# Optimization experiments

Hardware: AMD Instinct MI355X
Metric: run time of the kernel (lower is better)

Reference implementation:

```python
import jax, jax.numpy as jnp
import numpy as np

N_QUBITS = 12
DEPTH = 1
OUTPUT_DIM = 4096
BATCH = 2048
M = 4096  # input dim == 2**N_QUBITS, amplitude embedding needs no padding
EPS = 1e-10


def _rot_matrix(phi, theta, omega):
    """PennyLane qml.Rot(phi, theta, omega) = RZ(omega) @ RY(theta) @ RZ(phi)."""
    c = jnp.cos(theta * 0.5).astype(jnp.complex64)
    s = jnp.sin(theta * 0.5).astype(jnp.complex64)
    e_mm = jnp.exp(-0.5j * (phi + omega))  # e^{-i(phi+omega)/2}
    e_pm = jnp.exp(0.5j * (phi - omega))   # e^{+i(phi-omega)/2}
    e_mp = jnp.exp(0.5j * (omega - phi))   # e^{+i(omega-phi)/2}
    e_pp = jnp.exp(0.5j * (phi + omega))   # e^{+i(phi+omega)/2}
    return jnp.stack([
        jnp.stack([e_mm * c, -e_pm * s]),
        jnp.stack([e_mp * s, e_pp * c]),
    ])  # [2, 2] complex64


def _apply_1q(state, U, wire):
    """Apply 2x2 gate U on `wire` (MSB-first convention, as PennyLane)."""
    B = state.shape[0]
    s = state.reshape(B, 2 ** wire, 2, -1)
    return jnp.einsum('ij,bajc->baic', U, s).reshape(B, -1)


def _apply_cnot(state, ctrl, tgt):
    """Apply CNOT with control ctrl < target tgt (MSB-first wires)."""
    B = state.shape[0]
    s = state.reshape(B, 2 ** ctrl, 2, 2 ** (tgt - ctrl - 1), 2, -1)
    flipped = s[:, :, 1, :, ::-1, :]  # flip target axis where control == 1
    s = jnp.concatenate([s[:, :, :1], flipped[:, :, None]], axis=2)
    return s.reshape(B, -1)


def _circuit(x, w):
    # amplitude embedding: per-sample L2 normalize, uniform fallback for ~zero rows
    norm = jnp.linalg.norm(x, axis=1, keepdims=True)  # [B, 1]
    amp = jnp.where(norm > EPS, x / jnp.maximum(norm, EPS), 1.0 / np.sqrt(M))
    state = amp.astype(jnp.complex64)  # [B, 2^12]
    for layer in range(DEPTH):
        for i in range(N_QUBITS):
            U = _rot_matrix(w[layer, i, 0], w[layer, i, 1], w[layer, i, 2])
            state = _apply_1q(state, U, i)
        for i in range(N_QUBITS):
            for j in range(i + 1, N_QUBITS):
                state = _apply_cnot(state, i, j)
    probs = state.real ** 2 + state.imag ** 2  # [B, 4096]
    probs_n = probs[:, :OUTPUT_DIM]
    ps = probs_n.sum(axis=1, keepdims=True)
    out = jnp.where(ps > EPS, probs_n / jnp.maximum(ps, EPS), 1.0 / OUTPUT_DIM)
    return out.astype(jnp.float32)


def setup_inputs() -> dict:
    key = jax.random.key(0)
    k1, k2 = jax.random.split(key)
    x = jax.random.normal(k1, (BATCH, M), dtype=jnp.float32)
    quantum_weights = jax.random.uniform(
        k2, (DEPTH, N_QUBITS, 3), dtype=jnp.float32) * (2.0 * np.pi)
    return {"x": x, "quantum_weights": quantum_weights}


def reference(x, quantum_weights):
    return _circuit(x, quantum_weights)
```

## Files before the change

### kernel.cpp

```cpp
#include <hip/hip_runtime.h>
#include <math.h>


#define EPSF 1e-10f

__device__ __forceinline__ float dpp_xor1(float v) {
    return __int_as_float(__builtin_amdgcn_update_dpp(
        0, __float_as_int(v), 0xB1, 0xF, 0xF, true));
}
__device__ __forceinline__ float dpp_xor2(float v) {
    return __int_as_float(__builtin_amdgcn_update_dpp(
        0, __float_as_int(v), 0x4E, 0xF, 0xF, true));
}

__global__ __launch_bounds__(256, 4) void qdense_kernel(
    const float* __restrict__ x,
    const float* __restrict__ qw,
    float* __restrict__ out)
{
    __shared__ __align__(16) float buf[8192];
    __shared__ float bsum[4];

    const int tid = threadIdx.x;
    const int w   = tid >> 6;
    const int ln  = tid & 63;
    const int row = blockIdx.x;

    const float* __restrict__ xr = x + ((size_t)row << 12);

    float ar[16], ai[16];

    float ss = 0.f;
    const int wl = (w << 6) | ln;
#pragma unroll
    for (int l = 0; l < 16; ++l) {
        const float v = xr[(l << 8) | wl];
        ar[l] = v;
        ss = fmaf(v, v, ss);
    }
#pragma unroll
    for (int m = 32; m; m >>= 1) ss += __shfl_xor(ss, m, 64);
    if (ln == 0) bsum[w] = ss;
    __syncthreads();
    const float ss_tot = bsum[0] + bsum[1] + bsum[2] + bsum[3];

    const float nrm = sqrtf(ss_tot);
    if (nrm > EPSF) {
        const float inv = 1.0f / nrm;
#pragma unroll
        for (int l = 0; l < 16; ++l) ar[l] *= inv;
    } else {
#pragma unroll
        for (int l = 0; l < 16; ++l) ar[l] = 0.015625f;
    }
#pragma unroll
    for (int l = 0; l < 16; ++l) ai[l] = 0.f;

#define COEFFS(wq)                                                   \
    const float phi = qw[(wq) * 3 + 0];                              \
    const float th  = qw[(wq) * 3 + 1];                              \
    const float om  = qw[(wq) * 3 + 2];                              \
    const float c = __cosf(0.5f * th), s = __sinf(0.5f * th);        \
    const float A = 0.5f * (phi + om), Bb = 0.5f * (phi - om);       \
    const float p = c * __cosf(A), q = c * __sinf(A);                \
    const float r = s * __cosf(Bb), t = s * __sinf(Bb);

#pragma unroll
    for (int wq = 0; wq < 4; ++wq) {
        COEFFS(wq);
        const int bit = 1 << (3 - wq);
#pragma unroll
        for (int l0 = 0; l0 < 16; ++l0) {
            if (l0 & bit) continue;
            const int l1 = l0 | bit;
            const float a0r = ar[l0], a0i = ai[l0];
            const float a1r = ar[l1], a1i = ai[l1];
            ar[l0] =  p * a0r + q * a0i - r * a1r + t * a1i;
            ai[l0] = -q * a0r + p * a0i - t * a1r - r * a1i;
            ar[l1] =  r * a0r + t * a0i + p * a1r - q * a1i;
            ai[l1] = -t * a0r + r * a0i + q * a1r + p * a1i;
        }
    }

#pragma unroll
    for (int wq = 10; wq <= 11; ++wq) {
        COEFFS(wq);
        const int pb = 11 - wq;
        const int side = (ln >> pb) & 1;
        const float sq = side ? -q : q;
        const float sr = side ? r : -r;
#pragma unroll
        for (int l = 0; l < 16; ++l) {
            const float pr = (pb == 0) ? dpp_xor1(ar[l]) : dpp_xor2(ar[l]);
            const float pi = (pb == 0) ? dpp_xor1(ai[l]) : dpp_xor2(ai[l]);
            const float mr = ar[l], mi = ai[l];
            ar[l] = p * mr + sq * mi + sr * pr + t * pi;
            ai[l] = p * mi - sq * mr - t * pr + sr * pi;
        }
    }

    float2* __restrict__ B2 = reinterpret_cast<float2*>(buf);
#pragma unroll
    for (int l = 0; l < 16; ++l)
        B2[(l << 8) | (w << 6) | (ln ^ (l << 2))] = make_float2(ar[l], ai[l]);
    __syncthreads();
    {
        const int lo = (ln >> 2) & 15;
#pragma unroll
        for (int l2 = 0; l2 < 16; ++l2) {
            const int la = ((l2 << 2) | (ln & 3)) ^ (lo << 2);
            const float2 v = B2[(lo << 8) | (w << 6) | la];
            ar[l2] = v.x; ai[l2] = v.y;
        }
    }

#pragma unroll
    for (int wq = 6; wq < 10; ++wq) {
        COEFFS(wq);
        const int bit = 1 << (9 - wq);
#pragma unroll
        for (int l0 = 0; l0 < 16; ++l0) {
            if (l0 & bit) continue;
            const int l1 = l0 | bit;
            const float a0r = ar[l0], a0i = ai[l0];
            const float a1r = ar[l1], a1i = ai[l1];
            ar[l0] =  p * a0r + q * a0i - r * a1r + t * a1i;
            ai[l0] = -q * a0r + p * a0i - t * a1r - r * a1i;
            ar[l1] =  r * a0r + t * a0i + p * a1r - q * a1i;
            ai[l1] = -t * a0r + r * a0i + q * a1r + p * a1i;
        }
    }

#pragma unroll
    for (int wq = 4; wq <= 5; ++wq) {
        COEFFS(wq);
        const int wmask = (wq == 4) ? 2 : 1;
        const int side  = (w & wmask) ? 1 : 0;
        const float sq = side ? -q : q;
        const float sr = side ? r : -r;
        const int pw = w ^ wmask;
        __syncthreads();
#pragma unroll
        for (int l = 0; l < 16; ++l)
            B2[(l << 8) | (w << 6) | ln] = make_float2(ar[l], ai[l]);
        __syncthreads();
#pragma unroll
        for (int l = 0; l < 16; ++l) {
            const float2 pp = B2[(l << 8) | (pw << 6) | ln];
            const float mr = ar[l], mi = ai[l];
            ar[l] = p * mr + sq * mi + sr * pp.x + t * pp.y;
            ai[l] = p * mi - sq * mr - t * pp.x + sr * pp.y;
        }
    }

    float p2[16];
    float s2 = 0.f;
#pragma unroll
    for (int l = 0; l < 16; ++l) {
        p2[l] = fmaf(ar[l], ar[l], ai[l] * ai[l]);
        s2 += p2[l];
    }
#pragma unroll
    for (int m = 32; m; m >>= 1) s2 += __shfl_xor(s2, m, 64);

    __syncthreads();
    if (ln == 0) bsum[w] = s2;
    {
        const int hi = ((ln >> 2) & 15) << 8;
#pragma unroll
        for (int l2 = 0; l2 < 16; ++l2) {
            const int sdx = hi | (w << 6) | (l2 << 2) | (ln & 3);
            const int g   = sdx ^ (sdx >> 1);
            buf[g ^ (((g >> 8) & 7) << 2)] = p2[l2];
        }
    }
    __syncthreads();

    const float ps = bsum[0] + bsum[1] + bsum[2] + bsum[3];
    float* __restrict__ orow = out + ((size_t)row << 12);
    if (ps > EPSF) {
        const float sc = 1.0f / ps;
#pragma unroll
        for (int v = 0; v < 4; ++v) {
            const int k   = (w << 10) | (v << 8) | (ln << 2);
            const int idx = k ^ (((k >> 8) & 7) << 2);
            float4 d = *reinterpret_cast<const float4*>(&buf[idx]);
            d.x *= sc; d.y *= sc; d.z *= sc; d.w *= sc;
            *reinterpret_cast<float4*>(&orow[k]) = d;
        }
    } else {
        const float u = 1.0f / 4096.0f;
        const float4 d = make_float4(u, u, u, u);
#pragma unroll
        for (int v = 0; v < 4; ++v) {
            const int k = (w << 10) | (v << 8) | (ln << 2);
            *reinterpret_cast<float4*>(&orow[k]) = d;
        }
    }
}

extern "C" void kernel_launch(void* const* d_in, const int* in_sizes, int n_in,
                              void* d_out, int out_size, void* d_ws, size_t ws_size,
                              hipStream_t stream) {
    const float* x  = (const float*)d_in[0];
    const float* qw = (const float*)d_in[1];
    float* out = (float*)d_out;
    qdense_kernel<<<2048, 256, 0, stream>>>(x, qw, out);
}
```

Before: 119.2 us.

## Halve LDS footprint with staged exchanges and use packed FP32 complex math

Shared memory drops from 32 KB to 16 KB by running the transposition and cross-wave gate exchanges in two halves, each with extra barriers. Launch bounds rise to 8 blocks per CU to allow higher occupancy. Amplitudes are stored as float2 vectors and updated with packed FMAs (v_pk_fma_f32) to cut the ALU instruction count. The cost is more __syncthreads calls, with waves idling in the serialized transpose phases, plus possible register pressure under the tighter launch bound.

Result: faster. 106.0 us (-11.1%).

```diff
diff --git a/kernel.cpp b/kernel.cpp
--- a/kernel.cpp
+++ b/kernel.cpp
@@ -3,6 +3,8 @@
 
 
 #define EPSF 1e-10f
+
+typedef float f32x2 __attribute__((ext_vector_type(2)));
 
 __device__ __forceinline__ float dpp_xor1(float v) {
     return __int_as_float(__builtin_amdgcn_update_dpp(
@@ -12,14 +14,19 @@
     return __int_as_float(__builtin_amdgcn_update_dpp(
         0, __float_as_int(v), 0x4E, 0xF, 0xF, true));
 }
-
-__global__ __launch_bounds__(256, 4) void qdense_kernel(
+__device__ __forceinline__ f32x2 swp(f32x2 v) { return f32x2{v.y, v.x}; }
+__device__ __forceinline__ f32x2 pkfma(f32x2 a, f32x2 b, f32x2 c) {
+    return __builtin_elementwise_fma(a, b, c);
+}
+
+__global__ __launch_bounds__(256, 8) void qdense_kernel(
     const float* __restrict__ x,
     const float* __restrict__ qw,
     float* __restrict__ out)
 {
-    __shared__ __align__(16) float buf[8192];
+    __shared__ __align__(16) float buf[4096];
     __shared__ float bsum[4];
+    f32x2* __restrict__ B2 = reinterpret_cast<f32x2*>(buf);
 
     const int tid = threadIdx.x;
     const int w   = tid >> 6;
@@ -28,14 +35,14 @@
 
     const float* __restrict__ xr = x + ((size_t)row << 12);
 
-    float ar[16], ai[16];
+    f32x2 a[16];
 
     float ss = 0.f;
     const int wl = (w << 6) | ln;
 #pragma unroll
     for (int l = 0; l < 16; ++l) {
         const float v = xr[(l << 8) | wl];
-        ar[l] = v;
+        a[l].x = v; a[l].y = 0.f;
         ss = fmaf(v, v, ss);
     }
 #pragma unroll
@@ -48,13 +55,11 @@
     if (nrm > EPSF) {
         const float inv = 1.0f / nrm;
 #pragma unroll
-        for (int l = 0; l < 16; ++l) ar[l] *= inv;
+        for (int l = 0; l < 16; ++l) a[l].x *= inv;
     } else {
 #pragma unroll
-        for (int l = 0; l < 16; ++l) ar[l] = 0.015625f;
-    }
-#pragma unroll
-    for (int l = 0; l < 16; ++l) ai[l] = 0.f;
+        for (int l = 0; l < 16; ++l) a[l].x = 0.015625f;
+    }
 
 #define COEFFS(wq)                                                   \
     const float phi = qw[(wq) * 3 + 0];                              \
@@ -68,17 +73,15 @@
 #pragma unroll
     for (int wq = 0; wq < 4; ++wq) {
         COEFFS(wq);
+        const f32x2 P={p,p}, Q={q,-q}, Qm={-q,q}, R={r,r}, Rm={-r,-r}, T={t,-t};
         const int bit = 1 << (3 - wq);
 #pragma unroll
         for (int l0 = 0; l0 < 16; ++l0) {
             if (l0 & bit) continue;
             const int l1 = l0 | bit;
-            const float a0r = ar[l0], a0i = ai[l0];
-            const float a1r = ar[l1], a1i = ai[l1];
-            ar[l0] =  p * a0r + q * a0i - r * a1r + t * a1i;
-            ai[l0] = -q * a0r + p * a0i - t * a1r - r * a1i;
-            ar[l1] =  r * a0r + t * a0i + p * a1r - q * a1i;
-            ai[l1] = -t * a0r + r * a0i + q * a1r + p * a1i;
+            const f32x2 u0 = a[l0], u1 = a[l1], s0 = swp(u0), s1 = swp(u1);
+            a[l0] = pkfma(P, u0, pkfma(Q, s0, pkfma(Rm, u1, T * s1)));
+            a[l1] = pkfma(R, u0, pkfma(T, s0, pkfma(P, u1, Qm * s1)));
         }
     }
 
@@ -89,45 +92,48 @@
         const int side = (ln >> pb) & 1;
         const float sq = side ? -q : q;
         const float sr = side ? r : -r;
+        const f32x2 P={p,p}, Sq={sq,-sq}, Sr={sr,sr}, Tv={t,-t};
 #pragma unroll
         for (int l = 0; l < 16; ++l) {
-            const float pr = (pb == 0) ? dpp_xor1(ar[l]) : dpp_xor2(ar[l]);
-            const float pi = (pb == 0) ? dpp_xor1(ai[l]) : dpp_xor2(ai[l]);
-            const float mr = ar[l], mi = ai[l];
-            ar[l] = p * mr + sq * mi + sr * pr + t * pi;
-            ai[l] = p * mi - sq * mr - t * pr + sr * pi;
-        }
-    }
-
-    float2* __restrict__ B2 = reinterpret_cast<float2*>(buf);
-#pragma unroll
-    for (int l = 0; l < 16; ++l)
-        B2[(l << 8) | (w << 6) | (ln ^ (l << 2))] = make_float2(ar[l], ai[l]);
-    __syncthreads();
-    {
-        const int lo = (ln >> 2) & 15;
-#pragma unroll
-        for (int l2 = 0; l2 < 16; ++l2) {
-            const int la = ((l2 << 2) | (ln & 3)) ^ (lo << 2);
-            const float2 v = B2[(lo << 8) | (w << 6) | la];
-            ar[l2] = v.x; ai[l2] = v.y;
-        }
+            const f32x2 m = a[l];
+            f32x2 pp;
+            pp.x = (pb == 0) ? dpp_xor1(m.x) : dpp_xor2(m.x);
+            pp.y = (pb == 0) ? dpp_xor1(m.y) : dpp_xor2(m.y);
+            a[l] = pkfma(P, m, pkfma(Sq, swp(m), pkfma(Sr, pp, Tv * swp(pp))));
+        }
+    }
+
+#pragma unroll
+    for (int c = 0; c < 2; ++c) {
+        if ((w >> 1) == c) {
+#pragma unroll
+            for (int l = 0; l < 16; ++l)
+                B2[(l << 7) | ((w & 1) << 6) | ((ln ^ (l << 2)) & 63)] = a[l];
+        }
+        __syncthreads();
+        if ((w >> 1) == c) {
+            const int lo = (ln >> 2) & 15;
+#pragma unroll
+            for (int l2 = 0; l2 < 16; ++l2) {
+                const int la = (((l2 << 2) | (ln & 3)) ^ (lo << 2)) & 63;
+                a[l2] = B2[(lo << 7) | ((w & 1) << 6) | la];
+            }
+        }
+        __syncthreads();
     }
 
 #pragma unroll
     for (int wq = 6; wq < 10; ++wq) {
         COEFFS(wq);
+        const f32x2 P={p,p}, Q={q,-q}, Qm={-q,q}, R={r,r}, Rm={-r,-r}, T={t,-t};
         const int bit = 1 << (9 - wq);
 #pragma unroll
         for (int l0 = 0; l0 < 16; ++l0) {
             if (l0 & bit) continue;
             const int l1 = l0 | bit;
-            const float a0r = ar[l0], a0i = ai[l0];
-            const float a1r = ar[l1], a1i = ai[l1];
-            ar[l0] =  p * a0r + q * a0i - r * a1r + t * a1i;
-            ai[l0] = -q * a0r + p * a0i - t * a1r - r * a1i;
-            ar[l1] =  r * a0r + t * a0i + p * a1r - q * a1i;
-            ai[l1] = -t * a0r + r * a0i + q * a1r + p * a1i;
+            const f32x2 u0 = a[l0], u1 = a[l1], s0 = swp(u0), s1 = swp(u1);
+            a[l0] = pkfma(P, u0, pkfma(Q, s0, pkfma(Rm, u1, T * s1)));
+            a[l1] = pkfma(R, u0, pkfma(T, s0, pkfma(P, u1, Qm * s1)));
         }
     }
 
@@ -138,42 +144,42 @@
         const int side  = (w & wmask) ? 1 : 0;
         const float sq = side ? -q : q;
         const float sr = side ? r : -r;
+        const f32x2 P={p,p}, Sq={sq,-sq}, Sr={sr,sr}, Tv={t,-t};
         const int pw = w ^ wmask;
-        __syncthreads();
-#pragma unroll
-        for (int l = 0; l < 16; ++l)
-            B2[(l << 8) | (w << 6) | ln] = make_float2(ar[l], ai[l]);
-        __syncthreads();
-#pragma unroll
-        for (int l = 0; l < 16; ++l) {
-            const float2 pp = B2[(l << 8) | (pw << 6) | ln];
-            const float mr = ar[l], mi = ai[l];
-            ar[l] = p * mr + sq * mi + sr * pp.x + t * pp.y;
-            ai[l] = p * mi - sq * mr - t * pp.x + sr * pp.y;
-        }
-    }
-
-    float p2[16];
+#pragma unroll
+        for (int c2 = 0; c2 < 2; ++c2) {
+#pragma unroll
+            for (int rr = 0; rr < 8; ++rr) {
+                const int l = (c2 << 3) | rr;
+                B2[(rr << 8) | (w << 6) | ln] = a[l];
+            }
+            __syncthreads();
+#pragma unroll
+            for (int rr = 0; rr < 8; ++rr) {
+                const int l = (c2 << 3) | rr;
+                const f32x2 pp = B2[(rr << 8) | (pw << 6) | ln];
+                const f32x2 m = a[l];
+                a[l] = pkfma(P, m, pkfma(Sq, swp(m), pkfma(Sr, pp, Tv * swp(pp))));
+            }
+            __syncthreads();
+        }
+    }
+
     float s2 = 0.f;
-#pragma unroll
-    for (int l = 0; l < 16; ++l) {
-        p2[l] = fmaf(ar[l], ar[l], ai[l] * ai[l]);
-        s2 += p2[l];
-    }
-#pragma unroll
-    for (int m = 32; m; m >>= 1) s2 += __shfl_xor(s2, m, 64);
-
-    __syncthreads();
-    if (ln == 0) bsum[w] = s2;
     {
         const int hi = ((ln >> 2) & 15) << 8;
 #pragma unroll
         for (int l2 = 0; l2 < 16; ++l2) {
+            const float pr2 = fmaf(a[l2].x, a[l2].x, a[l2].y * a[l2].y);
+            s2 += pr2;
             const int sdx = hi | (w << 6) | (l2 << 2) | (ln & 3);
             const int g   = sdx ^ (sdx >> 1);
-            buf[g ^ (((g >> 8) & 7) << 2)] = p2[l2];
-        }
-    }
+            buf[g ^ (((g >> 8) & 7) << 2)] = pr2;
+        }
+    }
+#pragma unroll
+    for (int m = 32; m; m >>= 1) s2 += __shfl_xor(s2, m, 64);
+    if (ln == 0) bsum[w] = s2;
     __syncthreads();
 
     const float ps = bsum[0] + bsum[1] + bsum[2] + bsum[3];
```
